# Kernel tuning notes

Measured on AMD Instinct MI355X. Metric: run time of the kernel, lower is better.

## Reference

```python
import jax, jax.numpy as jnp
import numpy as np

N_ITER = 5          # n_iterations
EPS_VAR = 1e-6      # added to var (both in update_likelihoods and after M-step)
EPS = 1e-7          # division guard in M-step


def setup_inputs() -> dict:
    key = jax.random.key(0)
    B, N, K, F = 8, 80000, 5, 20
    k1, k2 = jax.random.split(key)
    data = jax.random.normal(k1, (B, N, F), dtype=jnp.float32)
    # initialize_parameters: means are randomly sampled data points
    idx = jax.random.randint(k2, (B, K), 0, N)
    means = jnp.take_along_axis(data, idx[:, :, None], axis=1)          # [B,K,F]
    variance = jnp.ones((B, K, F), dtype=jnp.float32)                    # covariance_init=1.0
    prior = jnp.full((B, K), 1.0 / K, dtype=jnp.float32)
    return {"data": data, "means": means, "variance": variance, "prior": prior}


def _log_likelihoods(data, means, var, pi):
    # data [B,N,F], means/var [B,K,F], pi [B,K] -> [B,K,N]
    inv_cov = 1.0 / (var + EPS_VAR)                                       # [B,K,F]
    diff = data[:, None, :, :] - means[:, :, None, :]                     # [B,K,N,F]
    maha = jnp.einsum('bknf,bkf->bkn', diff * diff, inv_cov)              # bmm in torch
    coeff = -0.5 * jnp.log(2.0 * np.pi * var).sum(axis=-1)                # [B,K]
    return jnp.log(pi)[:, :, None] + coeff[:, :, None] - 0.5 * maha


def _posteriors(log_lik):
    # stable softmax over the cluster dim (dim=1), identical to update_posteriors
    return jax.nn.softmax(log_lik, axis=1)


def _m_step(post, data):
    # post [B,K,N], data [B,N,F]; weights == 1.0 branch of update_parameters
    n = data.shape[1]
    sizes = post.sum(axis=2, keepdims=True)                               # [B,K,1] cluster sizes
    pi = sizes[..., 0] / n                                                # [B,K]
    pi = pi / jnp.maximum(jnp.abs(pi).sum(axis=-1, keepdims=True), 1e-12) # L1 normalize
    means = jnp.einsum('bkn,bnf->bkf', post, data) / (sizes + EPS)        # [B,K,F]
    diff = data[:, None, :, :] - means[:, :, None, :]                     # [B,K,N,F]
    var = jnp.einsum('bkn,bknf->bkf', post, diff * diff) / (sizes + EPS)
    return means, var, pi


def reference(data, means, variance, prior):
    var, pi = variance, prior
    for _ in range(N_ITER):
        ll = _log_likelihoods(data, means, var, pi)
        post = _posteriors(ll)
        means, var, pi = _m_step(post, data)
        var = var + EPS_VAR
    ll = _log_likelihoods(data, means, var, pi)
    post = _posteriors(ll)
    # outputs permuted to [B, N, K] as in forward()
    return (jnp.transpose(ll, (0, 2, 1)), jnp.transpose(post, (0, 2, 1)), means, var, pi)
```

## Files before the change

### kernel.cpp

```cpp
#include <hip/hip_runtime.h>
#include <math.h>

#define BB 8
#define NPTS 80000
#define KK 5
#define FF 20
#define GG 128
#define TILE 64
#define NTILES (NPTS / TILE)
#define PSTRIDE 48

#define WS_CM 0
#define WS_CV 800
#define WS_CP 1600
#define WS_A  1640
#define WS_D  1680
#define WS_E  2480

__device__ __forceinline__ void make_coefs(const float* __restrict__ means,
                                           const float* __restrict__ var,
                                           const float* __restrict__ pi,
                                           float* __restrict__ A, float* __restrict__ D,
                                           float* __restrict__ E, int t) {
    if (t < BB * KK) {
        float sumlog = 0.f, summ2 = 0.f;
        for (int f = 0; f < FF; ++f) {
            float v = var[t * FF + f];
            float m = means[t * FF + f];
            float ic = 1.f / (v + 1e-6f);
            sumlog += logf(6.283185307179586f * v);
            summ2  += ic * m * m;
            D[t * FF + f] = ic * m;
            E[t * FF + f] = -0.5f * ic;
        }
        A[t] = logf(pi[t]) - 0.5f * sumlog - 0.5f * summ2;
    }
}

__global__ void prepare_kernel(const float* __restrict__ means, const float* __restrict__ var,
                               const float* __restrict__ pi, float* __restrict__ ws) {
    make_coefs(means, var, pi, ws + WS_A, ws + WS_D, ws + WS_E, (int)threadIdx.x);
}

template <bool WRITE_OUT>
__global__ __launch_bounds__(320) void estep_kernel(const float* __restrict__ data,
                                                    const float* __restrict__ ws,
                                                    float* __restrict__ partials,
                                                    float* __restrict__ out_ll,
                                                    float* __restrict__ out_post) {
    __shared__ float xs[FF][TILE + 1];
    __shared__ float lls[KK][TILE];

    const int b    = blockIdx.x / GG;
    const int g    = blockIdx.x % GG;
    const int tid  = threadIdx.x;
    const int w    = __builtin_amdgcn_readfirstlane(tid >> 6);
    const int lane = tid & 63;
    const int sp   = (tid * 4) / FF;
    const int sf   = (tid * 4) % FF;

    const float* A = ws + WS_A;
    const float* D = ws + WS_D;
    const float* E = ws + WS_E;

    const float Ak = A[b * KK + w];
    float dk[FF], ek[FF];
#pragma unroll
    for (int f = 0; f < FF; ++f) {
        dk[f] = D[(b * KK + w) * FF + f];
        ek[f] = E[(b * KK + w) * FF + f];
    }

    float s0 = 0.f, s1[FF], s2[FF];
    if (!WRITE_OUT) {
#pragma unroll
        for (int f = 0; f < FF; ++f) { s1[f] = 0.f; s2[f] = 0.f; }
    }

    const float* dbase = data + (size_t)b * NPTS * FF;

    float4 v = ((const float4*)(dbase + (size_t)g * TILE * FF))[tid];
    for (int t = g; t < NTILES; t += GG) {
        const int tn = t + GG;
        float4 vn = v;
        if (tn < NTILES) vn = ((const float4*)(dbase + (size_t)tn * TILE * FF))[tid];

        xs[sf][sp] = v.x; xs[sf + 1][sp] = v.y; xs[sf + 2][sp] = v.z; xs[sf + 3][sp] = v.w;
        __syncthreads();

        float x[FF];
        float z = Ak;
#pragma unroll
        for (int f = 0; f < FF; ++f) {
            x[f] = xs[f][lane];
            z += x[f] * fmaf(ek[f], x[f], dk[f]);
        }
        lls[w][lane] = z;
        __syncthreads();

        float l0 = lls[0][lane], l1 = lls[1][lane], l2 = lls[2][lane],
              l3 = lls[3][lane], l4 = lls[4][lane];
        float mx = fmaxf(fmaxf(fmaxf(l0, l1), fmaxf(l2, l3)), l4);
        float e0 = __expf(l0 - mx), e1 = __expf(l1 - mx), e2 = __expf(l2 - mx),
              e3 = __expf(l3 - mx), e4 = __expf(l4 - mx);
        float inv = 1.f / (e0 + e1 + e2 + e3 + e4);
        float ew  = (w == 0) ? e0 : (w == 1) ? e1 : (w == 2) ? e2 : (w == 3) ? e3 : e4;
        float post = ew * inv;

        if (WRITE_OUT) {
            size_t o = ((size_t)b * NPTS + (size_t)t * TILE + lane) * KK + w;
            out_ll[o]   = z;
            out_post[o] = post;
        } else {
            s0 += post;
#pragma unroll
            for (int f = 0; f < FF; ++f) {
                float px = post * x[f];
                s1[f] += px;
                s2[f] += px * x[f];
            }
        }
        v = vn;
    }

    if (!WRITE_OUT) {
#pragma unroll
        for (int off = 32; off > 0; off >>= 1) {
            s0 += __shfl_down(s0, off);
#pragma unroll
            for (int f = 0; f < FF; ++f) {
                s1[f] += __shfl_down(s1[f], off);
                s2[f] += __shfl_down(s2[f], off);
            }
        }
        if (lane == 0) {
            float* row = partials + ((size_t)(b * KK + w) * GG + g) * PSTRIDE;
#pragma unroll
            for (int f = 0; f < FF; ++f) { row[f] = s1[f]; row[FF + f] = s2[f]; }
            row[2 * FF] = s0;
        }
    }
}

__global__ __launch_bounds__(320) void update_kernel(const float* __restrict__ partials,
                                                     float* __restrict__ ws,
                                                     float* __restrict__ om,
                                                     float* __restrict__ ov,
                                                     float* __restrict__ op,
                                                     int write_params) {
    __shared__ float s0s[KK];
    const int b    = blockIdx.x;
    const int tid  = threadIdx.x;
    const int w    = tid >> 6;
    const int lane = tid & 63;
    const int bk   = b * KK + w;

    float sv = 0.f;
    if (lane < PSTRIDE) {
        const float* base = partials + (size_t)bk * GG * PSTRIDE + lane;
        for (int gg = 0; gg < GG; ++gg) sv += base[(size_t)gg * PSTRIDE];
    }
    float s0  = __shfl(sv, 2 * FF);
    float den = s0 + 1e-7f;
    float m   = sv / den;
    float s2f = __shfl(sv, FF + (lane % FF));
    float var = (s2f - 2.f * m * sv + m * m * s0) / den + 1e-6f;

    float* cm = ws + WS_CM; float* cv = ws + WS_CV; float* cp = ws + WS_CP;
    if (lane < FF) {
        cm[bk * FF + lane] = m;
        cv[bk * FF + lane] = var;
        if (write_params) { om[bk * FF + lane] = m; ov[bk * FF + lane] = var; }
    }

    if (lane == 0) s0s[w] = s0;
    __syncthreads();
    float tot = s0s[0] + s0s[1] + s0s[2] + s0s[3] + s0s[4];
    float pr  = (s0 / (float)NPTS) / fmaxf(tot / (float)NPTS, 1e-12f);
    if (lane == 0) {
        cp[bk] = pr;
        if (write_params) op[bk] = pr;
    }

    float ic = 1.f / (var + 1e-6f);
    if (lane < FF) {
        (ws + WS_D)[bk * FF + lane] = ic * m;
        (ws + WS_E)[bk * FF + lane] = -0.5f * ic;
    }
    float t1 = (lane < FF) ? logf(6.283185307179586f * var) : 0.f;
    float t2 = (lane < FF) ? ic * m * m : 0.f;
#pragma unroll
    for (int off = 1; off < 64; off <<= 1) {
        t1 += __shfl_xor(t1, off);
        t2 += __shfl_xor(t2, off);
    }
    if (lane == 0)
        (ws + WS_A)[bk] = logf(pr) - 0.5f * t1 - 0.5f * t2;
}

extern "C" void kernel_launch(void* const* d_in, const int* in_sizes, int n_in,
                              void* d_out, int out_size, void* d_ws, size_t ws_size,
                              hipStream_t stream) {
    const float* data     = (const float*)d_in[0];
    const float* in_means = (const float*)d_in[1];
    const float* in_var   = (const float*)d_in[2];
    const float* in_pi    = (const float*)d_in[3];
    float* ws  = (float*)d_ws;
    float* out = (float*)d_out;

    float* out_ll   = out;
    float* out_post = out + (size_t)BB * NPTS * KK;
    float* om       = out + 2 * (size_t)BB * NPTS * KK;
    float* ov       = om + BB * KK * FF;
    float* op       = ov + BB * KK * FF;

    float* partials = out_ll;

    prepare_kernel<<<1, 64, 0, stream>>>(in_means, in_var, in_pi, ws);

    for (int it = 0; it < 5; ++it) {
        estep_kernel<false><<<BB * GG, 320, 0, stream>>>(data, ws, partials,
                                                         nullptr, nullptr);
        update_kernel<<<BB, 320, 0, stream>>>(partials, ws, om, ov, op,
                                              (it == 4) ? 1 : 0);
    }
    estep_kernel<true><<<BB * GG, 320, 0, stream>>>(data, ws, nullptr,
                                                    out_ll, out_post);
}
```

Before: 283.1 us.

## Double-buffer E-step tiles with deeper prefetch and even tile split

Changes the grid split to 125 groups per batch so each block gets exactly 10 tiles. The E-step now uses double-buffered shared memory with a two-tile-ahead register prefetch, cutting one barrier per tile. The update kernel's partial-sum reduction uses four independent accumulators to expose load parallelism. The extra buffering raises shared memory and register use, and there are slightly fewer blocks.

```diff
diff --git a/kernel.cpp b/kernel.cpp
--- a/kernel.cpp
+++ b/kernel.cpp
@@ -5,9 +5,10 @@
 #define NPTS 80000
 #define KK 5
 #define FF 20
-#define GG 128
+#define GG 125
 #define TILE 64
 #define NTILES (NPTS / TILE)
+#define JT (NTILES / GG)
 #define PSTRIDE 48
 
 #define WS_CM 0
@@ -48,8 +49,8 @@
                                                     float* __restrict__ partials,
                                                     float* __restrict__ out_ll,
                                                     float* __restrict__ out_post) {
-    __shared__ float xs[FF][TILE + 1];
-    __shared__ float lls[KK][TILE];
+    __shared__ float xs[2][FF][TILE + 1];
+    __shared__ float lls[2][KK][TILE];
 
     const int b    = blockIdx.x / GG;
     const int g    = blockIdx.x % GG;
@@ -59,16 +60,12 @@
     const int sp   = (tid * 4) / FF;
     const int sf   = (tid * 4) % FF;
 
-    const float* A = ws + WS_A;
-    const float* D = ws + WS_D;
-    const float* E = ws + WS_E;
-
-    const float Ak = A[b * KK + w];
+    const float Ak = (ws + WS_A)[b * KK + w];
     float dk[FF], ek[FF];
 #pragma unroll
     for (int f = 0; f < FF; ++f) {
-        dk[f] = D[(b * KK + w) * FF + f];
-        ek[f] = E[(b * KK + w) * FF + f];
+        dk[f] = (ws + WS_D)[(b * KK + w) * FF + f];
+        ek[f] = (ws + WS_E)[(b * KK + w) * FF + f];
     }
 
     float s0 = 0.f, s1[FF], s2[FF];
@@ -78,28 +75,37 @@
     }
 
     const float* dbase = data + (size_t)b * NPTS * FF;
-
-    float4 v = ((const float4*)(dbase + (size_t)g * TILE * FF))[tid];
-    for (int t = g; t < NTILES; t += GG) {
-        const int tn = t + GG;
-        float4 vn = v;
-        if (tn < NTILES) vn = ((const float4*)(dbase + (size_t)tn * TILE * FF))[tid];
-
-        xs[sf][sp] = v.x; xs[sf + 1][sp] = v.y; xs[sf + 2][sp] = v.z; xs[sf + 3][sp] = v.w;
-        __syncthreads();
+    #define TPTR(j) ((const float4*)(dbase + (size_t)(g + (j) * GG) * TILE * FF))
+
+    float4 v0 = TPTR(0)[tid];
+    float4 v  = TPTR(1)[tid];
+    float4 v2 = TPTR(2)[tid];
+    xs[0][sf][sp] = v0.x; xs[0][sf + 1][sp] = v0.y;
+    xs[0][sf + 2][sp] = v0.z; xs[0][sf + 3][sp] = v0.w;
+    __syncthreads();
+
+    int cur = 0;
+    for (int j = 0; j < JT; ++j) {
+        const int nxt = cur ^ 1;
+        if (j + 1 < JT) {
+            xs[nxt][sf][sp] = v.x; xs[nxt][sf + 1][sp] = v.y;
+            xs[nxt][sf + 2][sp] = v.z; xs[nxt][sf + 3][sp] = v.w;
+        }
+        v = v2;
+        if (j + 3 < JT) v2 = TPTR(j + 3)[tid];
 
         float x[FF];
         float z = Ak;
 #pragma unroll
         for (int f = 0; f < FF; ++f) {
-            x[f] = xs[f][lane];
+            x[f] = xs[cur][f][lane];
             z += x[f] * fmaf(ek[f], x[f], dk[f]);
         }
-        lls[w][lane] = z;
+        lls[cur][w][lane] = z;
         __syncthreads();
 
-        float l0 = lls[0][lane], l1 = lls[1][lane], l2 = lls[2][lane],
-              l3 = lls[3][lane], l4 = lls[4][lane];
+        float l0 = lls[cur][0][lane], l1 = lls[cur][1][lane], l2 = lls[cur][2][lane],
+              l3 = lls[cur][3][lane], l4 = lls[cur][4][lane];
         float mx = fmaxf(fmaxf(fmaxf(l0, l1), fmaxf(l2, l3)), l4);
         float e0 = __expf(l0 - mx), e1 = __expf(l1 - mx), e2 = __expf(l2 - mx),
               e3 = __expf(l3 - mx), e4 = __expf(l4 - mx);
@@ -108,7 +114,7 @@
         float post = ew * inv;
 
         if (WRITE_OUT) {
-            size_t o = ((size_t)b * NPTS + (size_t)t * TILE + lane) * KK + w;
+            size_t o = ((size_t)b * NPTS + (size_t)(g + j * GG) * TILE + lane) * KK + w;
             out_ll[o]   = z;
             out_post[o] = post;
         } else {
@@ -120,8 +126,9 @@
                 s2[f] += px * x[f];
             }
         }
-        v = vn;
-    }
+        cur = nxt;
+    }
+    #undef TPTR
 
     if (!WRITE_OUT) {
 #pragma unroll
@@ -155,11 +162,20 @@
     const int lane = tid & 63;
     const int bk   = b * KK + w;
 
-    float sv = 0.f;
+    float a0 = 0.f, a1 = 0.f, a2 = 0.f, a3 = 0.f;
     if (lane < PSTRIDE) {
         const float* base = partials + (size_t)bk * GG * PSTRIDE + lane;
-        for (int gg = 0; gg < GG; ++gg) sv += base[(size_t)gg * PSTRIDE];
-    }
+        int gg = 0;
+        for (; gg + 4 <= GG; gg += 4) {
+            a0 += base[(size_t)(gg + 0) * PSTRIDE];
+            a1 += base[(size_t)(gg + 1) * PSTRIDE];
+            a2 += base[(size_t)(gg + 2) * PSTRIDE];
+            a3 += base[(size_t)(gg + 3) * PSTRIDE];
+        }
+        for (; gg < GG; ++gg) a0 += base[(size_t)gg * PSTRIDE];
+    }
+    float sv = (a0 + a1) + (a2 + a3);
+
     float s0  = __shfl(sv, 2 * FF);
     float den = s0 + 1e-7f;
     float m   = sv / den;
```

New measurement: 326.3 us. 1.15x slower.

## Compute all clusters per lane and split accumulation across two waves

Applied to the files above, without the earlier changes.

Each lane now loads its whole point straight from global memory and computes all five cluster log-likelihoods itself. This removes the shared-memory transpose and both block barriers, and stops the per-wave recomputation of the softmax. The block shrinks to two waves that split the five clusters' sufficient statistics (2+3), coefficients are interleaved per batch for scalar loads, and partial reductions stop at 8 sub-rows per block. The cost is that the update kernel has to sum more partial rows, and register pressure is high with up to 3×41 accumulators per lane.

```diff
diff --git a/kernel.cpp b/kernel.cpp
--- a/kernel.cpp
+++ b/kernel.cpp
@@ -5,24 +5,21 @@
 #define NPTS 80000
 #define KK 5
 #define FF 20
-#define GG 128
+#define GG 125
 #define TILE 64
 #define NTILES (NPTS / TILE)
-#define PSTRIDE 48
-
-#define WS_CM 0
-#define WS_CV 800
-#define WS_CP 1600
-#define WS_A  1640
-#define WS_D  1680
-#define WS_E  2480
-
-__device__ __forceinline__ void make_coefs(const float* __restrict__ means,
-                                           const float* __restrict__ var,
-                                           const float* __restrict__ pi,
-                                           float* __restrict__ A, float* __restrict__ D,
-                                           float* __restrict__ E, int t) {
+#define JT (NTILES / GG)
+#define RSUB 8
+#define PR 44
+
+#define WS_A 0
+#define WS_R 64
+
+__global__ void prepare_kernel(const float* __restrict__ means, const float* __restrict__ var,
+                               const float* __restrict__ pi, float* __restrict__ ws) {
+    int t = threadIdx.x;
     if (t < BB * KK) {
+        int b = t / KK, k = t % KK;
         float sumlog = 0.f, summ2 = 0.f;
         for (int f = 0; f < FF; ++f) {
             float v = var[t * FF + f];
@@ -30,114 +27,156 @@
             float ic = 1.f / (v + 1e-6f);
             sumlog += logf(6.283185307179586f * v);
             summ2  += ic * m * m;
-            D[t * FF + f] = ic * m;
-            E[t * FF + f] = -0.5f * ic;
-        }
-        A[t] = logf(pi[t]) - 0.5f * sumlog - 0.5f * summ2;
-    }
-}
-
-__global__ void prepare_kernel(const float* __restrict__ means, const float* __restrict__ var,
-                               const float* __restrict__ pi, float* __restrict__ ws) {
-    make_coefs(means, var, pi, ws + WS_A, ws + WS_D, ws + WS_E, (int)threadIdx.x);
-}
-
-template <bool WRITE_OUT>
-__global__ __launch_bounds__(320) void estep_kernel(const float* __restrict__ data,
-                                                    const float* __restrict__ ws,
-                                                    float* __restrict__ partials,
-                                                    float* __restrict__ out_ll,
-                                                    float* __restrict__ out_post) {
-    __shared__ float xs[FF][TILE + 1];
-    __shared__ float lls[KK][TILE];
-
+            float* R = ws + WS_R + (b * FF + f) * 10;
+            R[k]     = ic * m;
+            R[5 + k] = -0.5f * ic;
+        }
+        (ws + WS_A)[t] = logf(pi[t]) - 0.5f * sumlog - 0.5f * summ2;
+    }
+}
+
+template <int KLO, int NK>
+__device__ __forceinline__ void estep_acc_wave(const float* __restrict__ dbase,
+                                               const float* cf, const float* __restrict__ Ab,
+                                               int b, int g, int lane,
+                                               float* __restrict__ partials) {
+    const float A0 = Ab[0], A1 = Ab[1], A2 = Ab[2], A3 = Ab[3], A4 = Ab[4];
+    float s0[NK], s1[NK][FF], s2[NK][FF];
+#pragma unroll
+    for (int q = 0; q < NK; ++q) {
+        s0[q] = 0.f;
+#pragma unroll
+        for (int f = 0; f < FF; ++f) { s1[q][f] = 0.f; s2[q][f] = 0.f; }
+    }
+
+    for (int j = 0; j < JT; ++j) {
+        asm volatile("" : "+s"(cf));
+        const int tile = g + j * GG;
+        const float4* tp = (const float4*)(dbase + (size_t)tile * TILE * FF);
+        float4 x4[5];
+#pragma unroll
+        for (int i = 0; i < 5; ++i) x4[i] = tp[lane * 5 + i];
+        float xv[FF];
+#pragma unroll
+        for (int i = 0; i < 5; ++i) {
+            xv[i * 4 + 0] = x4[i].x; xv[i * 4 + 1] = x4[i].y;
+            xv[i * 4 + 2] = x4[i].z; xv[i * 4 + 3] = x4[i].w;
+        }
+        float z0 = A0, z1 = A1, z2 = A2, z3 = A3, z4 = A4;
+#pragma unroll
+        for (int f = 0; f < FF; ++f) {
+            const float* r = cf + f * 10;
+            float x = xv[f];
+            z0 = fmaf(x, fmaf(r[5], x, r[0]), z0);
+            z1 = fmaf(x, fmaf(r[6], x, r[1]), z1);
+            z2 = fmaf(x, fmaf(r[7], x, r[2]), z2);
+            z3 = fmaf(x, fmaf(r[8], x, r[3]), z3);
+            z4 = fmaf(x, fmaf(r[9], x, r[4]), z4);
+        }
+        float mx = fmaxf(fmaxf(fmaxf(z0, z1), fmaxf(z2, z3)), z4);
+        float e0 = __expf(z0 - mx), e1 = __expf(z1 - mx), e2 = __expf(z2 - mx),
+              e3 = __expf(z3 - mx), e4 = __expf(z4 - mx);
+        float inv = 1.f / (e0 + e1 + e2 + e3 + e4);
+        float ev[5] = {e0, e1, e2, e3, e4};
+#pragma unroll
+        for (int q = 0; q < NK; ++q) {
+            float p = ev[KLO + q] * inv;
+            s0[q] += p;
+#pragma unroll
+            for (int f = 0; f < FF; ++f) {
+                float px = p * xv[f];
+                s1[q][f] += px;
+                s2[q][f] = fmaf(px, xv[f], s2[q][f]);
+            }
+        }
+    }
+
+#pragma unroll
+    for (int off = 32; off >= 8; off >>= 1) {
+#pragma unroll
+        for (int q = 0; q < NK; ++q) {
+            s0[q] += __shfl_down(s0[q], off);
+#pragma unroll
+            for (int f = 0; f < FF; ++f) {
+                s1[q][f] += __shfl_down(s1[q][f], off);
+                s2[q][f] += __shfl_down(s2[q][f], off);
+            }
+        }
+    }
+    if (lane < RSUB) {
+#pragma unroll
+        for (int q = 0; q < NK; ++q) {
+            float* row = partials + (((size_t)(b * KK + KLO + q) * GG + g) * RSUB + lane) * PR;
+#pragma unroll
+            for (int f = 0; f < FF; ++f) { row[f] = s1[q][f]; row[FF + f] = s2[q][f]; }
+            row[2 * FF] = s0[q];
+        }
+    }
+}
+
+__global__ __launch_bounds__(128) void estep_acc_kernel(const float* __restrict__ data,
+                                                        const float* __restrict__ ws,
+                                                        float* __restrict__ partials) {
     const int b    = blockIdx.x / GG;
     const int g    = blockIdx.x % GG;
-    const int tid  = threadIdx.x;
-    const int w    = __builtin_amdgcn_readfirstlane(tid >> 6);
-    const int lane = tid & 63;
-    const int sp   = (tid * 4) / FF;
-    const int sf   = (tid * 4) % FF;
-
-    const float* A = ws + WS_A;
-    const float* D = ws + WS_D;
-    const float* E = ws + WS_E;
-
-    const float Ak = A[b * KK + w];
-    float dk[FF], ek[FF];
-#pragma unroll
-    for (int f = 0; f < FF; ++f) {
-        dk[f] = D[(b * KK + w) * FF + f];
-        ek[f] = E[(b * KK + w) * FF + f];
-    }
-
-    float s0 = 0.f, s1[FF], s2[FF];
-    if (!WRITE_OUT) {
-#pragma unroll
-        for (int f = 0; f < FF; ++f) { s1[f] = 0.f; s2[f] = 0.f; }
-    }
-
+    const int wv   = threadIdx.x >> 6;
+    const int lane = threadIdx.x & 63;
+    const float* cf    = ws + WS_R + b * FF * 10;
+    const float* Ab    = ws + WS_A + b * KK;
     const float* dbase = data + (size_t)b * NPTS * FF;
-
-    float4 v = ((const float4*)(dbase + (size_t)g * TILE * FF))[tid];
-    for (int t = g; t < NTILES; t += GG) {
-        const int tn = t + GG;
-        float4 vn = v;
-        if (tn < NTILES) vn = ((const float4*)(dbase + (size_t)tn * TILE * FF))[tid];
-
-        xs[sf][sp] = v.x; xs[sf + 1][sp] = v.y; xs[sf + 2][sp] = v.z; xs[sf + 3][sp] = v.w;
-        __syncthreads();
-
-        float x[FF];
-        float z = Ak;
+    if (wv == 0) estep_acc_wave<0, 2>(dbase, cf, Ab, b, g, lane, partials);
+    else         estep_acc_wave<2, 3>(dbase, cf, Ab, b, g, lane, partials);
+}
+
+__global__ __launch_bounds__(128) void estep_write_kernel(const float* __restrict__ data,
+                                                          const float* __restrict__ ws,
+                                                          float* __restrict__ out_ll,
+                                                          float* __restrict__ out_post) {
+    const int b    = blockIdx.x / GG;
+    const int g    = blockIdx.x % GG;
+    const int wv   = threadIdx.x >> 6;
+    const int lane = threadIdx.x & 63;
+    const float* cf    = ws + WS_R + b * FF * 10;
+    const float* Ab    = ws + WS_A + b * KK;
+    const float* dbase = data + (size_t)b * NPTS * FF;
+    const float A0 = Ab[0], A1 = Ab[1], A2 = Ab[2], A3 = Ab[3], A4 = Ab[4];
+
+    for (int j = 0; j < JT; ++j) {
+        asm volatile("" : "+s"(cf));
+        const int tile = g + j * GG;
+        const float4* tp = (const float4*)(dbase + (size_t)tile * TILE * FF);
+        float4 x4[5];
+#pragma unroll
+        for (int i = 0; i < 5; ++i) x4[i] = tp[lane * 5 + i];
+        float xv[FF];
+#pragma unroll
+        for (int i = 0; i < 5; ++i) {
+            xv[i * 4 + 0] = x4[i].x; xv[i * 4 + 1] = x4[i].y;
+            xv[i * 4 + 2] = x4[i].z; xv[i * 4 + 3] = x4[i].w;
+        }
+        float z0 = A0, z1 = A1, z2 = A2, z3 = A3, z4 = A4;
 #pragma unroll
         for (int f = 0; f < FF; ++f) {
-            x[f] = xs[f][lane];
-            z += x[f] * fmaf(ek[f], x[f], dk[f]);
-        }
-        lls[w][lane] = z;
-        __syncthreads();
-
-        float l0 = lls[0][lane], l1 = lls[1][lane], l2 = lls[2][lane],
-              l3 = lls[3][lane], l4 = lls[4][lane];
-        float mx = fmaxf(fmaxf(fmaxf(l0, l1), fmaxf(l2, l3)), l4);
-        float e0 = __expf(l0 - mx), e1 = __expf(l1 - mx), e2 = __expf(l2 - mx),
-              e3 = __expf(l3 - mx), e4 = __expf(l4 - mx);
+            const float* r = cf + f * 10;
+            float x = xv[f];
+            z0 = fmaf(x, fmaf(r[5], x, r[0]), z0);
+            z1 = fmaf(x, fmaf(r[6], x, r[1]), z1);
+            z2 = fmaf(x, fmaf(r[7], x, r[2]), z2);
+            z3 = fmaf(x, fmaf(r[8], x, r[3]), z3);
+            z4 = fmaf(x, fmaf(r[9], x, r[4]), z4);
+        }
+        float mx = fmaxf(fmaxf(fmaxf(z0, z1), fmaxf(z2, z3)), z4);
+        float e0 = __expf(z0 - mx), e1 = __expf(z1 - mx), e2 = __expf(z2 - mx),
+              e3 = __expf(z3 - mx), e4 = __expf(z4 - mx);
         float inv = 1.f / (e0 + e1 + e2 + e3 + e4);
-        float ew  = (w == 0) ? e0 : (w == 1) ? e1 : (w == 2) ? e2 : (w == 3) ? e3 : e4;
-        float post = ew * inv;
-
-        if (WRITE_OUT) {
-            size_t o = ((size_t)b * NPTS + (size_t)t * TILE + lane) * KK + w;
-            out_ll[o]   = z;
-            out_post[o] = post;
+
+        size_t o = ((size_t)b * NPTS + (size_t)tile * TILE + lane) * KK;
+        if (wv == 0) {
+            out_ll[o + 0] = z0; out_ll[o + 1] = z1; out_ll[o + 2] = z2;
+            out_ll[o + 3] = z3; out_ll[o + 4] = z4;
         } else {
-            s0 += post;
-#pragma unroll
-            for (int f = 0; f < FF; ++f) {
-                float px = post * x[f];
-                s1[f] += px;
-                s2[f] += px * x[f];
-            }
-        }
-        v = vn;
-    }
-
-    if (!WRITE_OUT) {
-#pragma unroll
-        for (int off = 32; off > 0; off >>= 1) {
-            s0 += __shfl_down(s0, off);
-#pragma unroll
-            for (int f = 0; f < FF; ++f) {
-                s1[f] += __shfl_down(s1[f], off);
-                s2[f] += __shfl_down(s2[f], off);
-            }
-        }
-        if (lane == 0) {
-            float* row = partials + ((size_t)(b * KK + w) * GG + g) * PSTRIDE;
-#pragma unroll
-            for (int f = 0; f < FF; ++f) { row[f] = s1[f]; row[FF + f] = s2[f]; }
-            row[2 * FF] = s0;
+            out_post[o + 0] = e0 * inv; out_post[o + 1] = e1 * inv; out_post[o + 2] = e2 * inv;
+            out_post[o + 3] = e3 * inv; out_post[o + 4] = e4 * inv;
         }
     }
 }
@@ -155,37 +194,40 @@
     const int lane = tid & 63;
     const int bk   = b * KK + w;
 
-    float sv = 0.f;
-    if (lane < PSTRIDE) {
-        const float* base = partials + (size_t)bk * GG * PSTRIDE + lane;
-        for (int gg = 0; gg < GG; ++gg) sv += base[(size_t)gg * PSTRIDE];
-    }
+    float a0 = 0.f, a1 = 0.f, a2 = 0.f, a3 = 0.f;
+    if (lane < 2 * FF + 1) {
+        const float* base = partials + (size_t)bk * GG * RSUB * PR + lane;
+        for (int r = 0; r < GG * RSUB; r += 4) {
+            a0 += base[(size_t)(r + 0) * PR];
+            a1 += base[(size_t)(r + 1) * PR];
+            a2 += base[(size_t)(r + 2) * PR];
+            a3 += base[(size_t)(r + 3) * PR];
+        }
+    }
+    float sv = (a0 + a1) + (a2 + a3);
+
     float s0  = __shfl(sv, 2 * FF);
     float den = s0 + 1e-7f;
     float m   = sv / den;
     float s2f = __shfl(sv, FF + (lane % FF));
     float var = (s2f - 2.f * m * sv + m * m * s0) / den + 1e-6f;
 
-    float* cm = ws + WS_CM; float* cv = ws + WS_CV; float* cp = ws + WS_CP;
-    if (lane < FF) {
-        cm[bk * FF + lane] = m;
-        cv[bk * FF + lane] = var;
-        if (write_params) { om[bk * FF + lane] = m; ov[bk * FF + lane] = var; }
+    if (write_params && lane < FF) {
+        om[bk * FF + lane] = m;
+        ov[bk * FF + lane] = var;
     }
 
     if (lane == 0) s0s[w] = s0;
     __syncthreads();
     float tot = s0s[0] + s0s[1] + s0s[2] + s0s[3] + s0s[4];
     float pr  = (s0 / (float)NPTS) / fmaxf(tot / (float)NPTS, 1e-12f);
-    if (lane == 0) {
-        cp[bk] = pr;
-        if (write_params) op[bk] = pr;
-    }
+    if (write_params && lane == 0) op[bk] = pr;
 
     float ic = 1.f / (var + 1e-6f);
     if (lane < FF) {
-        (ws + WS_D)[bk * FF + lane] = ic * m;
-        (ws + WS_E)[bk * FF + lane] = -0.5f * ic;
+        float* R = ws + WS_R + (b * FF + lane) * 10;
+        R[w]     = ic * m;
+        R[5 + w] = -0.5f * ic;
     }
     float t1 = (lane < FF) ? logf(6.283185307179586f * var) : 0.f;
     float t2 = (lane < FF) ? ic * m * m : 0.f;
@@ -219,11 +261,9 @@
     prepare_kernel<<<1, 64, 0, stream>>>(in_means, in_var, in_pi, ws);
 
     for (int it = 0; it < 5; ++it) {
-        estep_kernel<false><<<BB * GG, 320, 0, stream>>>(data, ws, partials,
-                                                         nullptr, nullptr);
+        estep_acc_kernel<<<BB * GG, 128, 0, stream>>>(data, ws, partials);
         update_kernel<<<BB, 320, 0, stream>>>(partials, ws, om, ov, op,
                                               (it == 4) ? 1 : 0);
     }
-    estep_kernel<true><<<BB * GG, 320, 0, stream>>>(data, ws, nullptr,
-                                                    out_ll, out_post);
-}
+    estep_write_kernel<<<BB * GG, 128, 0, stream>>>(data, ws, out_ll, out_post);
+}
```

Result: slower. 455.2 us (+60.8%).
